# Optimization experiments

Hardware: AMD Instinct MI355X
Metric: run time of the kernel (lower is better)

Reference implementation:

```python
import jax, jax.numpy as jnp
import numpy as np

B, S, F = 4, 2048, 1024

def setup_inputs() -> dict:
    key = jax.random.key(0)
    ks = jax.random.split(key, 9)
    s = 1.0 / np.sqrt(F)
    return {
        "q": jax.random.normal(ks[0], (B, S, F), jnp.float32),
        "k": jax.random.normal(ks[1], (B, S, F), jnp.float32),
        "v": jax.random.normal(ks[2], (B, S, F), jnp.float32),
        "Wq": jax.random.normal(ks[3], (F, F), jnp.float32) * s,
        "bq": jax.random.normal(ks[4], (F,), jnp.float32) * s,
        "Wk": jax.random.normal(ks[5], (F, F), jnp.float32) * s,
        "bk": jax.random.normal(ks[6], (F,), jnp.float32) * s,
        "Wv": jax.random.normal(ks[7], (F, F), jnp.float32) * s,
        "bv": jax.random.normal(ks[8], (F,), jnp.float32) * s,
    }

def reference(q, k, v, Wq, bq, Wk, bk, Wv, bv):
    # Linear layers: x @ W^T + b (torch nn.Linear convention)
    qp = jnp.einsum('bsf,gf->bsg', q, Wq) + bq
    kp = jnp.einsum('bsf,gf->bsg', k, Wk) + bk
    vp = jnp.einsum('bsf,gf->bsg', v, Wv) + bv
    # Unscaled attention (no 1/sqrt(d)), as in the original module
    attn = jax.nn.softmax(jnp.einsum('bqf,bkf->bqk', qp, kp), axis=-1)
    return jnp.einsum('bqk,bkf->bqf', attn, vp) + q
```

## Files before the change

### kernel.cpp

```cpp
#include <hip/hip_runtime.h>

typedef unsigned short u16;
typedef __bf16 bf16x8 __attribute__((ext_vector_type(8)));
typedef float f32x4 __attribute__((ext_vector_type(4)));
typedef u16 u16x8 __attribute__((ext_vector_type(8)));

union B8 { u16x8 u; bf16x8 b; };

__device__ __forceinline__ u16 f2b(float f){
  unsigned u = __float_as_uint(f);
  return (u16)((u + 0x7FFFu + ((u >> 16) & 1u)) >> 16);
}
__device__ __forceinline__ float b2f(u16 h){ return __uint_as_float(((unsigned)h) << 16); }

__device__ __forceinline__ void gload16(const u16* g, u16* l){
  __builtin_amdgcn_global_load_lds((const __attribute__((address_space(1))) void*)g,
                                   (__attribute__((address_space(3))) void*)l, 16, 0, 0);
}

__global__ __launch_bounds__(256) void prep_kernel(
    const float* __restrict__ v, const float* __restrict__ Wv,
    const float* __restrict__ Wq, const float* __restrict__ Wk,
    const float* __restrict__ bq,
    u16* __restrict__ v_b, u16* __restrict__ Wv_b,
    u16* __restrict__ WqT_pair, u16* __restrict__ WkT_pair, float* __restrict__ b)
{
  __shared__ float lds[64][65];
  const int blk = blockIdx.x, t = threadIdx.x;
  if (blk < 4608){
    const float* src; u16* dst; long base;
    if (blk < 4096){ src = v;  dst = v_b;  base = blk; }
    else           { src = Wv; dst = Wv_b; base = blk - 4096; }
    long i = base * 256 + t;
    float4 x0 = ((const float4*)src)[2 * i];
    float4 x1 = ((const float4*)src)[2 * i + 1];
    float xs[8] = {x0.x, x0.y, x0.z, x0.w, x1.x, x1.y, x1.z, x1.w};
    u16x8 h;
    #pragma unroll
    for (int j = 0; j < 8; j++) h[j] = f2b(xs[j]);
    ((u16x8*)dst)[i] = h;
  } else if (blk < 5120){
    int tt = blk - 4608;
    const float* W = (tt >> 8) ? Wk : Wq;
    u16* outp      = (tt >> 8) ? WkT_pair : WqT_pair;
    int t16 = tt & 255, g0 = (t16 >> 4) * 64, f0 = (t16 & 15) * 64;
    int c4 = (t & 15) * 4, r0 = t >> 4;
    #pragma unroll
    for (int it = 0; it < 4; it++){
      int r = r0 + it * 16;
      float4 x = *(const float4*)&W[(long)(g0 + r) * 1024 + f0 + c4];
      lds[r][c4] = x.x; lds[r][c4+1] = x.y; lds[r][c4+2] = x.z; lds[r][c4+3] = x.w;
    }
    __syncthreads();
    #pragma unroll
    for (int it = 0; it < 2; it++){
      int task = t + it * 256;
      int fl = task >> 3, gi = task & 7;
      u16x8 h, l;
      #pragma unroll
      for (int jj = 0; jj < 8; jj++){
        float xv = lds[gi * 8 + jj][fl];
        h[jj] = f2b(xv); l[jj] = f2b(xv - b2f(h[jj]));
      }
      u16* o = outp + (long)(f0 + fl) * 2048 + ((g0 >> 3) + gi) * 16;
      *(u16x8*)o = h;
      *(u16x8*)(o + 8) = l;
    }
  } else {
    int e = (blk - 5120) * 256 + t;
    float acc = 0.f;
    for (int g = 0; g < 1024; g++) acc += Wk[(long)g * 1024 + e] * bq[g];
    b[e] = acc;
  }
}

__global__ __launch_bounds__(256) void split_qk_kernel(
    const float* __restrict__ q, const float* __restrict__ kk,
    const float* __restrict__ b,
    u16* __restrict__ q_pair, u16* __restrict__ k_pair, float* __restrict__ kb)
{
  const int blk = blockIdx.x, t = threadIdx.x;
  const bool isK = blk >= 4096;
  const float* src = isK ? kk : q;
  u16* dst = isK ? k_pair : q_pair;
  long base = isK ? blk - 4096 : blk;
  long i = base * 256 + t;
  float4 x0 = ((const float4*)src)[2 * i];
  float4 x1 = ((const float4*)src)[2 * i + 1];
  float xs[8] = {x0.x, x0.y, x0.z, x0.w, x1.x, x1.y, x1.z, x1.w};
  u16x8 h, l;
  #pragma unroll
  for (int j = 0; j < 8; j++){ h[j] = f2b(xs[j]); l[j] = f2b(xs[j] - b2f(h[j])); }
  ((u16x8*)dst)[2 * i]     = h;
  ((u16x8*)dst)[2 * i + 1] = l;
  if (isK){
    const int f = (t & 127) * 8;
    float d = 0.f;
    #pragma unroll
    for (int j = 0; j < 8; j++) d += xs[j] * b[f + j];
    #pragma unroll
    for (int off = 32; off > 0; off >>= 1) d += __shfl_xor(d, off, 64);
    __shared__ float red[4];
    if ((t & 63) == 0) red[t >> 6] = d;
    __syncthreads();
    if (t == 0)   kb[base * 2]     = red[0] + red[1];
    if (t == 128) kb[base * 2 + 1] = red[2] + red[3];
  }
}

__global__ __launch_bounds__(256) void reduce_split_kernel(
    const float* __restrict__ part, u16* __restrict__ out_pair, long nper)
{
  long i = (long)blockIdx.x * 256 + threadIdx.x;
  float s[8];
  #pragma unroll
  for (int j = 0; j < 8; j++) s[j] = 0.f;
  #pragma unroll
  for (int z = 0; z < 4; z++){
    float4 a0 = ((const float4*)(part + z * nper))[2 * i];
    float4 a1 = ((const float4*)(part + z * nper))[2 * i + 1];
    s[0]+=a0.x; s[1]+=a0.y; s[2]+=a0.z; s[3]+=a0.w;
    s[4]+=a1.x; s[5]+=a1.y; s[6]+=a1.z; s[7]+=a1.w;
  }
  u16x8 h, l;
  #pragma unroll
  for (int j = 0; j < 8; j++){ h[j] = f2b(s[j]); l[j] = f2b(s[j] - b2f(h[j])); }
  long e = (i * 8) >> 10;
  long g = i & 127;
  u16* o = out_pair + e * 2048 + g * 16;
  *(u16x8*)o = h;
  *(u16x8*)(o + 8) = l;
}

__device__ __forceinline__ void xcd_remap(int& tx, int& ty, int& tz){
  const int GX = gridDim.x, GY = gridDim.y;
  int b  = blockIdx.x + GX * (blockIdx.y + GY * blockIdx.z);
  int NB = GX * GY * gridDim.z;
  int rank = (b & 7) * (NB >> 3) + (b >> 3);
  int pz = GX * GY;
  tz = rank / pz;
  int r = rank - tz * pz;
  ty = r / GX;
  tx = r - ty * GX;
}

constexpr int BM = 128, BN = 128, BK = 32;

__device__ __forceinline__ int lds1_idx(int row, int g){ return row * 32 + g * 8; }
__device__ __forceinline__ int lds2_idx(int row, int g){
  return row * 64 + (((g ^ (row & 7)) & 7) << 3);
}

template<bool DUAL, int EPI>
__global__ __launch_bounds__(256, 4)
void gemm_nt(const u16* __restrict__ A, const u16* __restrict__ Bm,
             const float* __restrict__ bias, const float* __restrict__ residual,
             void* __restrict__ out0,
             int M, int N, int K, int Krow,
             long sAb, long sBb, long sOb, long sRb, int seq)
{
  constexpr int RW = DUAL ? 64 : 32;
  __shared__ u16 lds[2][BM * RW];

  int tx, ty, tz; xcd_remap(tx, ty, tz);
  const int t = threadIdx.x;
  const int tileM = ty * BM;
  const int tileN = tx * BN;
  const long rs = DUAL ? 2L * Krow : (long)Krow;

  const u16* gA = A  + tz * sAb + (long)tileM * rs;
  const u16* gB = Bm + tz * sBb + (long)tileN * rs;

  const int wave = t >> 6, lane = t & 63;
  const int wm = (wave >> 1) * 64, wn = (wave & 1) * 64;
  const int lr = lane & 15;
  const int lg = lane >> 4;

  const u16 *pa, *pb;
  long jstride;
  int  ldsbase, ldsstep, nissue, kadv;
  if (DUAL){
    const int lr8 = lane >> 3, sl = lane & 7;
    const int g = sl ^ lr8;
    pa = gA + (long)(wave * 32 + lr8) * rs + g * 8;
    pb = gB + (long)(wave * 32 + lr8) * rs + g * 8;
    jstride = 8 * rs;
    ldsbase = (wave * 32) * 64; ldsstep = 8 * 64;
    nissue = 4; kadv = 64;
  } else {
    pa = gA + (long)(wave * 32 + (lane >> 2)) * rs + (lane & 3) * 8;
    pb = gB + (long)(wave * 32 + (lane >> 2)) * rs + (lane & 3) * 8;
    jstride = 16 * rs;
    ldsbase = (wave * 32) * 32; ldsstep = 16 * 32;
    nissue = 2; kadv = 32;
  }

  f32x4 acc[4][4] = {};

  for (int k0 = 0; k0 < K; k0 += BK){
    __syncthreads();
    #pragma unroll 4
    for (int j = 0; j < nissue; j++){
      gload16(pa + j * jstride, &lds[0][ldsbase + j * ldsstep]);
      gload16(pb + j * jstride, &lds[1][ldsbase + j * ldsstep]);
    }
    pa += kadv; pb += kadv;
    __syncthreads();

    if (DUAL){
      B8 ah[4], al[4], bh[4], bl[4];
      #pragma unroll
      for (int mt = 0; mt < 4; mt++){
        int row = wm + mt * 16 + lr;
        ah[mt].u = *(const u16x8*)&lds[0][lds2_idx(row, lg * 2)];
        al[mt].u = *(const u16x8*)&lds[0][lds2_idx(row, lg * 2 + 1)];
      }
      #pragma unroll
      for (int nt = 0; nt < 4; nt++){
        int row = wn + nt * 16 + lr;
        bh[nt].u = *(const u16x8*)&lds[1][lds2_idx(row, lg * 2)];
        bl[nt].u = *(const u16x8*)&lds[1][lds2_idx(row, lg * 2 + 1)];
      }
      #pragma unroll
      for (int mt = 0; mt < 4; mt++){
        #pragma unroll
        for (int nt = 0; nt < 4; nt++){
          acc[mt][nt] = __builtin_amdgcn_mfma_f32_16x16x32_bf16(ah[mt].b, bh[nt].b, acc[mt][nt], 0, 0, 0);
          acc[mt][nt] = __builtin_amdgcn_mfma_f32_16x16x32_bf16(ah[mt].b, bl[nt].b, acc[mt][nt], 0, 0, 0);
          acc[mt][nt] = __builtin_amdgcn_mfma_f32_16x16x32_bf16(al[mt].b, bh[nt].b, acc[mt][nt], 0, 0, 0);
        }
      }
    } else {
      B8 af[4], bf[4];
      #pragma unroll
      for (int mt = 0; mt < 4; mt++)
        af[mt].u = *(const u16x8*)&lds[0][lds1_idx(wm + mt * 16 + lr, lg)];
      #pragma unroll
      for (int nt = 0; nt < 4; nt++)
        bf[nt].u = *(const u16x8*)&lds[1][lds1_idx(wn + nt * 16 + lr, lg)];
      #pragma unroll
      for (int mt = 0; mt < 4; mt++)
        #pragma unroll
        for (int nt = 0; nt < 4; nt++)
          acc[mt][nt] = __builtin_amdgcn_mfma_f32_16x16x32_bf16(af[mt].b, bf[nt].b, acc[mt][nt], 0, 0, 0);
    }
  }

  const int rq = lg * 4;
  #pragma unroll
  for (int nt = 0; nt < 4; nt++){
    const int n = tileN + wn + nt * 16 + lr;
    float bv = 0.f;
    if (EPI <= 1 && bias) bv = bias[n];
    if (EPI == 2 && bias) bv = bias[(long)tz * N + n];
    #pragma unroll
    for (int mt = 0; mt < 4; mt++){
      #pragma unroll
      for (int r = 0; r < 4; r++){
        const int m = tileM + wm + mt * 16 + rq + r;
        float val = acc[mt][nt][r] + bv;
        if (EPI == 0){
          u16 h = f2b(val);
          u16* o = (u16*)out0 + (long)tz * sOb + (long)m * 2 * N + ((n >> 3) << 4) + (n & 7);
          o[0] = h;
          o[8] = f2b(val - b2f(h));
        } else if (EPI == 1){
          long idx = (long)(m / seq) * ((long)N * seq) + (long)n * seq + (m % seq);
          ((u16*)out0)[idx] = f2b(val);
        } else if (EPI == 2){
          ((float*)out0)[(long)tz * sOb + (long)m * N + n] = val;
        } else {
          float res = residual[(long)tz * sRb + (long)m * N + n];
          ((float*)out0)[(long)tz * sOb + (long)m * N + n] = val + res;
        }
      }
    }
  }
}

__global__ __launch_bounds__(256)
void softmax_kernel(const float* __restrict__ S, u16* __restrict__ P, int n){
  const long row = blockIdx.x;
  const float* r = S + row * (long)n;
  const int t = threadIdx.x;
  float v[8];
  float mx = -3.0e38f;
  #pragma unroll
  for (int i = 0; i < 8; i++){ v[i] = r[t + (i << 8)]; mx = fmaxf(mx, v[i]); }
  #pragma unroll
  for (int off = 32; off > 0; off >>= 1) mx = fmaxf(mx, __shfl_xor(mx, off, 64));
  __shared__ float red[8];
  const int wave = t >> 6;
  if ((t & 63) == 0) red[wave] = mx;
  __syncthreads();
  mx = fmaxf(fmaxf(red[0], red[1]), fmaxf(red[2], red[3]));
  float s = 0.f;
  #pragma unroll
  for (int i = 0; i < 8; i++){ v[i] = __expf(v[i] - mx); s += v[i]; }
  #pragma unroll
  for (int off = 32; off > 0; off >>= 1) s += __shfl_xor(s, off, 64);
  if ((t & 63) == 0) red[4 + wave] = s;
  __syncthreads();
  s = red[4] + red[5] + red[6] + red[7];
  const float inv = 1.f / s;
  u16* pr = P + row * (long)n;
  #pragma unroll
  for (int i = 0; i < 8; i++) pr[t + (i << 8)] = f2b(v[i] * inv);
}

extern "C" void kernel_launch(void* const* d_in, const int* in_sizes, int n_in,
                              void* d_out, int out_size, void* d_ws, size_t ws_size,
                              hipStream_t stream){
  (void)in_sizes; (void)n_in; (void)out_size; (void)ws_size;
  const float* q  = (const float*)d_in[0];
  const float* k  = (const float*)d_in[1];
  const float* v  = (const float*)d_in[2];
  const float* Wq = (const float*)d_in[3];
  const float* bq = (const float*)d_in[4];
  const float* Wk = (const float*)d_in[5];
  const float* Wv = (const float*)d_in[7];
  const float* bv = (const float*)d_in[8];
  float* out = (float*)d_out;

  const int B = 4, S = 2048, F = 1024;
  const long NSF = (long)B * S * F;
  const long NFF = (long)F * F;
  const long NSS = (long)B * S * S;

  char* w = (char*)d_ws;
  auto alloc = [&](long bytes) -> char* {
    char* p = w; w += (bytes + 255) & ~(long)255; return p;
  };
  u16*   tmp_pair = (u16*)alloc(2 * NSF * 2);
  u16*   k_pair   = (u16*)alloc(2 * NSF * 2);
  u16*   vpT      = (u16*)alloc(NSF * 2);
  float* kb       = (float*)alloc((long)B * S * 4);
  char* zone2 = alloc(NSS * 2 + NSS * 4);
  u16*   attn   = (u16*)zone2;
  float* scores = (float*)(zone2 + NSS * 2);
  u16*   q_pair   = (u16*)zone2;
  char*  z3       = zone2 + NSS * 2;
  u16*   v_b      = (u16*)z3;
  u16*   Wv_b     = (u16*)(z3 + NSF * 2);
  u16*   WqT_pair = (u16*)(z3 + NSF * 2 + NFF * 2);
  u16*   WkT_pair = WqT_pair + 2 * NFF;
  float* b_vec    = (float*)(WkT_pair + 2 * NFF);
  float* Mt_part  = (float*)((char*)b_vec + 4096);
  u16*   Mt_pair  = (u16*)((char*)Mt_part + 4 * NFF * 4);

  dim3 blk(256);

  prep_kernel<<<dim3(5124), blk, 0, stream>>>(
      v, Wv, Wq, Wk, bq, v_b, Wv_b, WqT_pair, WkT_pair, b_vec);

  split_qk_kernel<<<dim3(8192), blk, 0, stream>>>(q, k, b_vec, q_pair, k_pair, kb);

  gemm_nt<true, 2><<<dim3(F / BN, F / BM, 4), blk, 0, stream>>>(
      WkT_pair, WqT_pair, nullptr, nullptr, Mt_part,
      F, F, 256, F, 512, 512, NFF, 0, S);

  reduce_split_kernel<<<dim3(512), blk, 0, stream>>>(Mt_part, Mt_pair, NFF);

  gemm_nt<true, 0><<<dim3(F / BN, (B * S) / BM, 1), blk, 0, stream>>>(
      q_pair, Mt_pair, nullptr, nullptr, tmp_pair,
      B * S, F, F, F, 0, 0, 0, 0, S);

  gemm_nt<false, 1><<<dim3(F / BN, (B * S) / BM, 1), blk, 0, stream>>>(
      v_b, Wv_b, bv, nullptr, vpT,
      B * S, F, F, F, 0, 0, 0, 0, S);

  gemm_nt<true, 2><<<dim3(S / BN, S / BM, B), blk, 0, stream>>>(
      tmp_pair, k_pair, kb, nullptr, scores,
      S, S, F, F, (long)S * 2 * F, (long)S * 2 * F, (long)S * S, 0, S);

  softmax_kernel<<<dim3(B * S), blk, 0, stream>>>(scores, attn, S);

  gemm_nt<false, 3><<<dim3(F / BN, S / BM, B), blk, 0, stream>>>(
      attn, vpT, nullptr, q, out,
      S, F, S, S, (long)S * S, (long)F * S, (long)S * F, (long)S * F, S);
}
```

Before: 463.2 us.

## Transpose V-projection GEMM for coalesced stores, parallelize bias vector, raise occupancy

The bias vector Wk^T·bq was computed by 4 blocks with a serial 1024-length loop. It is now a separate wave-parallel kernel that reads the already-transposed bf16 hi/lo WkT pair and reduces with shuffles. The V projection GEMM is swapped to compute Wv·v^T, so the transposed vpT output is written along contiguous sequence positions, and the bias is indexed by row. Non-dual GEMMs get launch bounds of 8 blocks per CU, which may limit registers and cause spills. The V projection is also moved earlier in the stream, right after prep.

```diff
diff --git a/kernel.cpp b/kernel.cpp
--- a/kernel.cpp
+++ b/kernel.cpp
@@ -21,9 +21,8 @@
 __global__ __launch_bounds__(256) void prep_kernel(
     const float* __restrict__ v, const float* __restrict__ Wv,
     const float* __restrict__ Wq, const float* __restrict__ Wk,
-    const float* __restrict__ bq,
     u16* __restrict__ v_b, u16* __restrict__ Wv_b,
-    u16* __restrict__ WqT_pair, u16* __restrict__ WkT_pair, float* __restrict__ b)
+    u16* __restrict__ WqT_pair, u16* __restrict__ WkT_pair)
 {
   __shared__ float lds[64][65];
   const int blk = blockIdx.x, t = threadIdx.x;
@@ -39,7 +38,7 @@
     #pragma unroll
     for (int j = 0; j < 8; j++) h[j] = f2b(xs[j]);
     ((u16x8*)dst)[i] = h;
-  } else if (blk < 5120){
+  } else {
     int tt = blk - 4608;
     const float* W = (tt >> 8) ? Wk : Wq;
     u16* outp      = (tt >> 8) ? WkT_pair : WqT_pair;
@@ -66,12 +65,27 @@
       *(u16x8*)o = h;
       *(u16x8*)(o + 8) = l;
     }
-  } else {
-    int e = (blk - 5120) * 256 + t;
-    float acc = 0.f;
-    for (int g = 0; g < 1024; g++) acc += Wk[(long)g * 1024 + e] * bq[g];
-    b[e] = acc;
-  }
+  }
+}
+
+__global__ __launch_bounds__(256) void bvec_kernel(
+    const u16* __restrict__ WkT_pair, const float* __restrict__ bq, float* __restrict__ b)
+{
+  const int wave = threadIdx.x >> 6, lane = threadIdx.x & 63;
+  const int e = blockIdx.x * 4 + wave;
+  const u16* row = WkT_pair + (long)e * 2048;
+  float acc = 0.f;
+  #pragma unroll
+  for (int ii = 0; ii < 2; ii++){
+    int gi = lane * 2 + ii;
+    const u16* p = row + gi * 16;
+    #pragma unroll
+    for (int j = 0; j < 8; j++)
+      acc += (b2f(p[j]) + b2f(p[j + 8])) * bq[gi * 8 + j];
+  }
+  #pragma unroll
+  for (int off = 32; off > 0; off >>= 1) acc += __shfl_xor(acc, off, 64);
+  if (lane == 0) b[e] = acc;
 }
 
 __global__ __launch_bounds__(256) void split_qk_kernel(
@@ -152,7 +166,7 @@
 }
 
 template<bool DUAL, int EPI>
-__global__ __launch_bounds__(256, 4)
+__global__ __launch_bounds__(256, DUAL ? 4 : 8)
 void gemm_nt(const u16* __restrict__ A, const u16* __restrict__ Bm,
              const float* __restrict__ bias, const float* __restrict__ residual,
              void* __restrict__ out0,
@@ -251,7 +265,7 @@
   for (int nt = 0; nt < 4; nt++){
     const int n = tileN + wn + nt * 16 + lr;
     float bv = 0.f;
-    if (EPI <= 1 && bias) bv = bias[n];
+    if (EPI == 0 && bias) bv = bias[n];
     if (EPI == 2 && bias) bv = bias[(long)tz * N + n];
     #pragma unroll
     for (int mt = 0; mt < 4; mt++){
@@ -264,14 +278,15 @@
           u16* o = (u16*)out0 + (long)tz * sOb + (long)m * 2 * N + ((n >> 3) << 4) + (n & 7);
           o[0] = h;
           o[8] = f2b(val - b2f(h));
-        } else if (EPI == 1){
-          long idx = (long)(m / seq) * ((long)N * seq) + (long)n * seq + (m % seq);
-          ((u16*)out0)[idx] = f2b(val);
         } else if (EPI == 2){
           ((float*)out0)[(long)tz * sOb + (long)m * N + n] = val;
-        } else {
+        } else if (EPI == 3){
           float res = residual[(long)tz * sRb + (long)m * N + n];
           ((float*)out0)[(long)tz * sOb + (long)m * N + n] = val + res;
+        } else {
+          if (bias) val += bias[m];
+          long idx = (long)(n / seq) * ((long)M * seq) + (long)m * seq + (n % seq);
+          ((u16*)out0)[idx] = f2b(val);
         }
       }
     }
@@ -350,8 +365,14 @@
 
   dim3 blk(256);
 
-  prep_kernel<<<dim3(5124), blk, 0, stream>>>(
-      v, Wv, Wq, Wk, bq, v_b, Wv_b, WqT_pair, WkT_pair, b_vec);
+  prep_kernel<<<dim3(5120), blk, 0, stream>>>(
+      v, Wv, Wq, Wk, v_b, Wv_b, WqT_pair, WkT_pair);
+
+  bvec_kernel<<<dim3(256), blk, 0, stream>>>(WkT_pair, bq, b_vec);
+
+  gemm_nt<false, 4><<<dim3((B * S) / BN, F / BM, 1), blk, 0, stream>>>(
+      Wv_b, v_b, bv, nullptr, vpT,
+      F, B * S, F, F, 0, 0, 0, 0, S);
 
   split_qk_kernel<<<dim3(8192), blk, 0, stream>>>(q, k, b_vec, q_pair, k_pair, kb);
 
@@ -365,10 +386,6 @@
       q_pair, Mt_pair, nullptr, nullptr, tmp_pair,
       B * S, F, F, F, 0, 0, 0, 0, S);
 
-  gemm_nt<false, 1><<<dim3(F / BN, (B * S) / BM, 1), blk, 0, stream>>>(
-      v_b, Wv_b, bv, nullptr, vpT,
-      B * S, F, F, F, 0, 0, 0, 0, S);
-
   gemm_nt<true, 2><<<dim3(S / BN, S / BM, B), blk, 0, stream>>>(
       tmp_pair, k_pair, kb, nullptr, scores,
       S, S, F, F, (long)S * 2 * F, (long)S * 2 * F, (long)S * S, 0, S);
```

Result: slower. 986.5 us (+113.0%).
